# Performance work log

Hardware: AMD Instinct MI355X
Metric: run time of the kernel (lower is better)

## Reference

```python
import jax, jax.numpy as jnp
import numpy as np

N_NODES = 100000
N_EDGES = 3200000
DIMS = [32, 256, 1024, 1024, 256, 6]


def setup_inputs() -> dict:
    key = jax.random.key(0)
    ks = jax.random.split(key, 2 + 2 * 5)
    inp = {
        "x": jax.random.normal(ks[0], (N_NODES, DIMS[0]), dtype=jnp.float32),
        "edge_index": jax.random.randint(ks[1], (2, N_EDGES), 0, N_NODES, dtype=jnp.int64),
    }
    for i in range(5):
        fan_in, fan_out = DIMS[i], DIMS[i + 1]
        scale = (2.0 / (fan_in + fan_out)) ** 0.5  # glorot-ish
        inp[f"W{i+1}"] = jax.random.normal(ks[2 + 2 * i], (fan_in, fan_out), dtype=jnp.float32) * scale
        inp[f"b{i+1}"] = jnp.zeros((fan_out,), dtype=jnp.float32)
    return inp


def _gcn_forward(x, edge_index, Ws, bs):
    N = x.shape[0]
    # add self loops (PyG GCNConv default)
    loop = jnp.arange(N, dtype=edge_index.dtype)
    src = jnp.concatenate([edge_index[0], loop])
    dst = jnp.concatenate([edge_index[1], loop])
    # symmetric normalization: deg computed on target index (gcn_norm)
    deg = jax.ops.segment_sum(jnp.ones_like(dst, dtype=x.dtype), dst, num_segments=N)
    dinv = jnp.where(deg > 0, jax.lax.rsqrt(deg), 0.0)
    norm = (dinv[src] * dinv[dst])[:, None]  # [E+N, 1]

    def conv(h, W, b):
        h = h @ W                                    # dense linear
        msg = h[src] * norm                          # gather + scale
        agg = jax.ops.segment_sum(msg, dst, num_segments=N)  # scatter-add
        return agg + b

    h = x
    for i in range(4):
        h = jax.nn.relu(conv(h, Ws[i], bs[i]))
    return conv(h, Ws[4], bs[4])


def reference(x, edge_index, W1, b1, W2, b2, W3, b3, W4, b4, W5, b5):
    return _gcn_forward(x, edge_index, (W1, W2, W3, W4, W5), (b1, b2, b3, b4, b5))
```

## Files before the change

### kernel.cpp

```cpp
#include <hip/hip_runtime.h>

typedef unsigned char u8;
typedef unsigned short u16;
typedef unsigned int u32;
typedef __bf16 bf16_t;
typedef bf16_t bf16x8 __attribute__((ext_vector_type(8)));
typedef float f32x4 __attribute__((ext_vector_type(4)));
typedef float f32x2 __attribute__((ext_vector_type(2)));

#define LDS_PTR(p) ((__attribute__((address_space(3))) unsigned int*)(p))
#define GLB_PTR(p) ((const __attribute__((address_space(1))) unsigned int*)(p))

#define BSH 9
#define BCAP 32768

static __device__ __forceinline__ float bf2f(u16 h) {
  u32 u = ((u32)h) << 16;
  return __builtin_bit_cast(float, u);
}
static __device__ __forceinline__ u16 f2bf(float f) {
  u32 u = __builtin_bit_cast(u32, f);
  u += 0x7fffu + ((u >> 16) & 1u);
  return (u16)(u >> 16);
}

static __device__ __forceinline__ int xcd_swizzle(int wg, int nwg) {
  const int q = nwg >> 3, r = nwg & 7;
  const int xcd = wg & 7, pos = wg >> 3;
  return (xcd < r ? xcd * (q + 1) : r * (q + 1) + (xcd - r) * q) + pos;
}

__global__ void detect_kernel(const int* __restrict__ ei, const u16* __restrict__ x,
                              int* __restrict__ flags, int* __restrict__ zp, int zn) {
  __shared__ int cnt;
  if (threadIdx.x == 0) cnt = 0;
  __syncthreads();
  if (blockIdx.x == 0) {
    if (ei[1 + 2 * threadIdx.x] != 0) atomicAdd(&cnt, 1);
    __syncthreads();
    if (threadIdx.x == 0) flags[0] = (cnt == 0) ? 1 : 0;
  } else if (blockIdx.x == 1) {
    u32 u = x[threadIdx.x];
    u32 e = (u >> 7) & 0xFF;
    if (e >= 0x60 && e <= 0x83) atomicAdd(&cnt, 1);
    __syncthreads();
    if (threadIdx.x == 0) flags[1] = (cnt >= 240) ? 0 : 1;
  } else {
    for (int i = threadIdx.x; i < zn; i += 256) zp[i] = 0;
  }
}

static __device__ __forceinline__ int eidx(const void* ei, size_t i, int m) {
  return m ? (int)((const long long*)ei)[i] : ((const int*)ei)[i];
}

__global__ void zero_out_kernel(void* __restrict__ out, int n, const int* __restrict__ flags) {
  int i = blockIdx.x * 256 + threadIdx.x;
  if (i < n) {
    if (flags[1]) ((float*)out)[i] = 0.0f;
    else ((u16*)out)[i] = 0;
  }
}

struct CvtArgs {
  const void* src[10];
  u16* dst[10];
  int K[10];
  int N[10];
  int start[11];
};
__global__ void convert_all_kernel(CvtArgs a, const int* __restrict__ flags) {
  int idx = blockIdx.x * 256 + threadIdx.x;
  int f32 = flags[1];
#pragma unroll
  for (int t = 0; t < 10; ++t) {
    if (idx >= a.start[t] && idx < a.start[t + 1]) {
      int local = idx - a.start[t];
      int K = a.K[t], N = a.N[t];
      int k = local / N, n = local - k * N;
      float v = f32 ? ((const float*)a.src[t])[local] : bf2f(((const u16*)a.src[t])[local]);
      a.dst[t][(size_t)n * K + k] = f2bf(v);
    }
  }
}

__global__ __launch_bounds__(256) void bin_kernel(const void* __restrict__ ei,
                                                  int* __restrict__ gcur,
                                                  int2* __restrict__ pairs, int E, int Nn,
                                                  const int* __restrict__ flags, int nblk) {
  __shared__ int h[256];
  __shared__ int base[256];
  const int m = flags[0];
  const int nb = (Nn + (1 << BSH) - 1) >> BSH;
  const int per = (E + nblk - 1) / nblk;
  const int e0 = blockIdx.x * per;
  const int e1 = (e0 + per < E) ? e0 + per : E;
  for (int i = threadIdx.x; i < nb; i += 256) h[i] = 0;
  __syncthreads();
  for (int e = e0 + threadIdx.x; e < e1; e += 256) {
    int d = eidx(ei, (size_t)E + e, m);
    if ((u32)d < (u32)Nn) atomicAdd(&h[d >> BSH], 1);
  }
  __syncthreads();
  for (int i = threadIdx.x; i < nb; i += 256) {
    base[i] = atomicAdd(&gcur[i], h[i]);
    h[i] = 0;
  }
  __syncthreads();
  for (int e = e0 + threadIdx.x; e < e1; e += 256) {
    int d = eidx(ei, (size_t)E + e, m);
    if ((u32)d >= (u32)Nn) continue;
    int s = eidx(ei, (size_t)e, m);
    if ((u32)s >= (u32)Nn) s = 0;
    int b = d >> BSH;
    int p = base[b] + atomicAdd(&h[b], 1);
    if (p < BCAP) pairs[(size_t)b * BCAP + p] = make_int2(s, d);
  }
}

__global__ __launch_bounds__(256) void bucket_scan_kernel(const int* __restrict__ gcur,
                                                          int* __restrict__ gbase, int NB) {
  __shared__ int sd[256];
  int tid = threadIdx.x;
  int v = (tid < NB) ? gcur[tid] : 0;
  if (v > BCAP) v = BCAP;
  sd[tid] = v;
  __syncthreads();
  for (int s = 1; s < 256; s <<= 1) {
    int t = (tid >= s) ? sd[tid - s] : 0;
    __syncthreads();
    sd[tid] += t;
    __syncthreads();
  }
  if (tid < NB) gbase[tid] = sd[tid] - v;
}

__global__ __launch_bounds__(512) void bucket_finalize_kernel(
    const int2* __restrict__ pairs, const int* __restrict__ gcur,
    const int* __restrict__ gbase, int* __restrict__ rowp, float* __restrict__ dinv,
    int* __restrict__ csr, int Nn) {
  __shared__ int cnt[512];
  __shared__ int scn[512];
  const int b = blockIdx.x;
  const int n0 = b << BSH;
  const int tid = threadIdx.x;
  cnt[tid] = 0;
  __syncthreads();
  int tot = gcur[b];
  if (tot > BCAP) tot = BCAP;
  for (int i = tid; i < tot; i += 512) {
    int2 pr = pairs[(size_t)b * BCAP + i];
    atomicAdd(&cnt[pr.y - n0], 1);
  }
  __syncthreads();
  int myc = cnt[tid];
  scn[tid] = myc;
  __syncthreads();
  for (int s = 1; s < 512; s <<= 1) {
    int t = (tid >= s) ? scn[tid - s] : 0;
    __syncthreads();
    scn[tid] += t;
    __syncthreads();
  }
  const int node = n0 + tid;
  const int start = gbase[b] + scn[tid] - myc;
  if (node < Nn) {
    rowp[node] = start;
    dinv[node] = rsqrtf((float)(myc + 1));
    if (node == Nn - 1) rowp[Nn] = gbase[b] + scn[tid];
  }
  cnt[tid] = start;
  __syncthreads();
  for (int i = tid; i < tot; i += 512) {
    int2 pr = pairs[(size_t)b * BCAP + i];
    int p = atomicAdd(&cnt[pr.y - n0], 1);
    csr[p] = pr.x;
  }
}

template <int NPW, int ACT, bool SRCF, bool DSTF, bool EDGEW>
__global__ __launch_bounds__(256) void spmm_narrow_kernel(
    const void* __restrict__ Hb, void* __restrict__ Gb,
    const int* __restrict__ rowp, const int* __restrict__ csr,
    const float* __restrict__ dinv, const u16* __restrict__ bias,
    int relu, int Nn, int src_stride, int dst_stride, const int* __restrict__ flags) {
  constexpr int G = 64 / NPW;
  constexpr int B = 16;
  const int lane = threadIdx.x & 63;
  const int col = lane & (G - 1);
  const int node = blockIdx.x * 4 * NPW + (threadIdx.x >> 6) * NPW + (lane / G);
  const bool anode = node < Nn;
  const bool act = anode && (col < ACT);
  int sf32 = 0, of32 = 0;
  if (SRCF) sf32 = flags[1];
  if (DSTF) of32 = flags[1];
  const u16* Hs = (const u16*)Hb;
  const float* Hf = (const float*)Hb;

  int e0 = 0, cnt = 0;
  if (anode) {
    e0 = rowp[node];
    cnt = rowp[node + 1] - e0;
  }
  float acc = 0.0f;
  for (int jb = 0; jb < cnt; jb += B) {
    int s[B];
#pragma unroll
    for (int j = 0; j < B; ++j) {
      bool val = (jb + j) < cnt;
      s[j] = val ? csr[e0 + jb + j] : node;
    }
    float wv[B];
    if constexpr (EDGEW) {
#pragma unroll
      for (int j = 0; j < B; ++j) wv[j] = ((jb + j) < cnt) ? dinv[s[j]] : 0.0f;
    }
    float v[B];
#pragma unroll
    for (int j = 0; j < B; ++j) {
      bool val = act && ((jb + j) < cnt);
      size_t idx = (size_t)s[j] * src_stride + col;
      v[j] = val ? ((SRCF && sf32) ? Hf[idx] : bf2f(Hs[idx])) : 0.0f;
    }
#pragma unroll
    for (int j = 0; j < B; ++j) {
      if constexpr (EDGEW) acc += wv[j] * v[j];
      else acc += v[j];
    }
  }
  if (!act) return;
  const float wi = dinv[node];
  {
    size_t idx = (size_t)node * src_stride + col;
    float sv = (SRCF && sf32) ? Hf[idx] : bf2f(Hs[idx]);
    if constexpr (EDGEW) acc += wi * sv;
    else acc += sv;
  }
  float v = acc * wi;
  if (bias) v += bf2f(bias[col]);
  if (relu) v = fmaxf(v, 0.0f);
  size_t didx = (size_t)node * dst_stride + col;
  if (DSTF && of32) ((float*)Gb)[didx] = v;
  else ((u16*)Gb)[didx] = f2bf(v);
}

template <int W>
__global__ __launch_bounds__(256) void spmm_fp8_kernel(
    const u8* __restrict__ Hq, u16* __restrict__ Gout,
    const int* __restrict__ rowp, const int* __restrict__ csr,
    const float* __restrict__ dinv, int n0, int n1, int dst_stride) {
  constexpr int BPL = W / 64;
  constexpr int ND = BPL / 4;
  constexpr int B = (W == 1024) ? 8 : 16;
  const int lane = threadIdx.x & 63;
  const int node = __builtin_amdgcn_readfirstlane(n0 + blockIdx.x * 4 + (threadIdx.x >> 6));
  if (node >= n1) return;
  const int off = lane * BPL;
  f32x2 acc[2 * ND] = {};

  auto dec1 = [&](const u32* d) {
#pragma unroll
    for (int q = 0; q < ND; ++q) {
      f32x2 a = __builtin_amdgcn_cvt_pk_f32_fp8((int)d[q], false);
      f32x2 b = __builtin_amdgcn_cvt_pk_f32_fp8((int)d[q], true);
      acc[2 * q] += a;
      acc[2 * q + 1] += b;
    }
  };
  auto ldrow = [&](u32* v, int s) {
    const u8* p = Hq + (size_t)s * W + off;
    if constexpr (ND == 4) *(int4*)v = *(const int4*)p;
    else v[0] = *(const u32*)p;
  };

  const int e0 = rowp[node];
  const int cnt = rowp[node + 1] - e0;
  const int tot = cnt + 1;
  const int NB2 = (tot + B - 1) / B;
  const int NBF = NB2 - 1;

  u32 vA[B][ND], vB[B][ND];

  auto ldb_full = [&](u32 (*v)[ND], int k) {
    const int base = k * B;
    int s[B];
#pragma unroll
    for (int j = 0; j < B; ++j) s[j] = csr[e0 + base + j];
#pragma unroll
    for (int j = 0; j < B; ++j) ldrow(v[j], s[j]);
  };
  auto ldb_last = [&](u32 (*v)[ND]) {
    const int base = NBF * B;
#pragma unroll
    for (int j = 0; j < B; ++j) {
      const int i = base + j;
      if (i < tot) {
        int s = (i < cnt) ? csr[e0 + i] : node;
        ldrow(v[j], s);
      } else {
#pragma unroll
        for (int q = 0; q < ND; ++q) v[j][q] = 0u;
      }
    }
  };
  auto decfull = [&](u32 (*v)[ND]) {
#pragma unroll
    for (int j = 0; j < B; ++j) dec1(v[j]);
  };

  if (NB2 == 1) {
    ldb_last(vA);
    decfull(vA);
  } else {
    ldb_last(vA);
    ldb_full(vB, 0);
    int k = 1;
    while (k + 1 < NBF) {
      decfull(vA);
      ldb_full(vA, k);
      decfull(vB);
      ldb_full(vB, k + 1);
      k += 2;
    }
    if (k < NBF) {
      decfull(vA);
      ldb_full(vA, k);
      decfull(vB);
      decfull(vA);
    } else {
      decfull(vA);
      decfull(vB);
    }
  }

  const float wi = dinv[node];
  u32 d[2 * ND];
#pragma unroll
  for (int kk = 0; kk < 2 * ND; ++kk) {
    float v0 = acc[kk].x * wi, v1 = acc[kk].y * wi;
    d[kk] = (u32)f2bf(v0) | ((u32)f2bf(v1) << 16);
  }
  u16* gp = Gout + (size_t)(node - n0) * dst_stride + off;
  if constexpr (ND == 4) {
    ((int4*)gp)[0] = make_int4((int)d[0], (int)d[1], (int)d[2], (int)d[3]);
    ((int4*)gp)[1] = make_int4((int)d[4], (int)d[5], (int)d[6], (int)d[7]);
  } else {
    *(int2*)gp = make_int2((int)d[0], (int)d[1]);
  }
}

__global__ __launch_bounds__(256) void spmm_u8_kernel(
    const u8* __restrict__ Hq, u16* __restrict__ G,
    const int* __restrict__ rowp, const int* __restrict__ csr,
    const float* __restrict__ dinv, const u32* __restrict__ maxbits,
    const u16* __restrict__ bias, int relu, int Nn, int dst_stride) {
  constexpr int B = 16;
  const int lane = threadIdx.x & 63;
  const int node = __builtin_amdgcn_readfirstlane(blockIdx.x * 4 + (threadIdx.x >> 6));
  if (node >= Nn) return;
  const int off = lane * 4;
  float mx = __builtin_bit_cast(float, *maxbits);
  float sq = mx > 0.0f ? mx * (1.0f / 127.0f) : 0.0f;
  float a0 = 0.0f, a1 = 0.0f, a2 = 0.0f, a3 = 0.0f, wsum = 0.0f;

  auto dec1 = [&](u32 d, float w) {
    a0 += w * (float)(d & 0xffu);
    a1 += w * (float)((d >> 8) & 0xffu);
    a2 += w * (float)((d >> 16) & 0xffu);
    a3 += w * (float)(d >> 24);
    wsum += w;
  };
  auto ldrow = [&](u32* v, int s) { *v = *(const u32*)(Hq + (size_t)s * 256 + off); };

  const int e0 = rowp[node];
  const int cnt = rowp[node + 1] - e0;
  const int tot = cnt + 1;
  const int NB2 = (tot + B - 1) / B;
  const int NBF = NB2 - 1;

  u32 vA[B], vB[B];
  float wA[B], wB[B];

  auto ldb_full = [&](u32* v, float* wv, int k) {
    const int base = k * B;
    int s[B];
#pragma unroll
    for (int j = 0; j < B; ++j) s[j] = csr[e0 + base + j];
#pragma unroll
    for (int j = 0; j < B; ++j) wv[j] = dinv[s[j]];
#pragma unroll
    for (int j = 0; j < B; ++j) ldrow(&v[j], s[j]);
  };
  auto ldb_last = [&](u32* v, float* wv) {
    const int base = NBF * B;
#pragma unroll
    for (int j = 0; j < B; ++j) {
      const int i = base + j;
      if (i < tot) {
        int s = (i < cnt) ? csr[e0 + i] : node;
        wv[j] = dinv[s];
        ldrow(&v[j], s);
      } else {
        v[j] = 0u;
        wv[j] = 0.0f;
      }
    }
  };
  auto decfull = [&](u32* v, float* wv) {
#pragma unroll
    for (int j = 0; j < B; ++j) dec1(v[j], wv[j]);
  };

  if (NB2 == 1) {
    ldb_last(vA, wA);
    decfull(vA, wA);
  } else {
    ldb_last(vA, wA);
    ldb_full(vB, wB, 0);
    int k = 1;
    while (k + 1 < NBF) {
      decfull(vA, wA);
      ldb_full(vA, wA, k);
      decfull(vB, wB);
      ldb_full(vB, wB, k + 1);
      k += 2;
    }
    if (k < NBF) {
      decfull(vA, wA);
      ldb_full(vA, wA, k);
      decfull(vB, wB);
      decfull(vA, wA);
    } else {
      decfull(vA, wA);
      decfull(vB, wB);
    }
  }

  const float wi = dinv[node];
  float su[4] = {a0, a1, a2, a3};
  float vals[4];
#pragma unroll
  for (int k2 = 0; k2 < 4; ++k2) {
    float v = (su[k2] - 128.0f * wsum) * wi * sq;
    if (bias) v += bf2f(bias[off + k2]);
    if (relu) v = fmaxf(v, 0.0f);
    vals[k2] = v;
  }
  u32 d0 = (u32)f2bf(vals[0]) | ((u32)f2bf(vals[1]) << 16);
  u32 d1 = (u32)f2bf(vals[2]) | ((u32)f2bf(vals[3]) << 16);
  *(int2*)(G + (size_t)node * dst_stride + off) = make_int2((int)d0, (int)d1);
}

__global__ void quant_kernel(const u16* __restrict__ t4, u8* __restrict__ t4q,
                             const u32* __restrict__ maxbits, int n4) {
  int i = blockIdx.x * 256 + threadIdx.x;
  if (i >= n4) return;
  float mx = __builtin_bit_cast(float, *maxbits);
  float inv = mx > 0.0f ? 127.0f / mx : 0.0f;
  int2 v = ((const int2*)t4)[i];
  float f0 = bf2f((u16)(v.x & 0xffff)), f1 = bf2f((u16)((u32)v.x >> 16));
  float f2 = bf2f((u16)(v.y & 0xffff)), f3 = bf2f((u16)((u32)v.y >> 16));
  int q0 = (int)rintf(f0 * inv), q1 = (int)rintf(f1 * inv);
  int q2 = (int)rintf(f2 * inv), q3 = (int)rintf(f3 * inv);
  q0 = min(127, max(-127, q0)) + 128; q1 = min(127, max(-127, q1)) + 128;
  q2 = min(127, max(-127, q2)) + 128; q3 = min(127, max(-127, q3)) + 128;
  ((u32*)t4q)[i] = (u32)q0 | ((u32)q1 << 8) | ((u32)q2 << 16) | ((u32)q3 << 24);
}

__global__ __launch_bounds__(512) void gemm256_kernel(
    const u16* __restrict__ A, int lda, const u16* __restrict__ Bt, int ldb,
    u16* __restrict__ C, int ldc, const u16* __restrict__ bias,
    int M, int K, int relu, int fp8out, const float* __restrict__ rowscale) {
  extern __shared__ u16 lds[];
  u16* ldsA = lds;
  u16* ldsB = lds + 32768;
  const int tid = threadIdx.x;
  const int lane = tid & 63;
  const int wid = __builtin_amdgcn_readfirstlane(tid >> 6);
  const int wr = wid >> 2, wc = wid & 3;
  const int lr = lane & 15, lq = lane >> 4;
  const int gx = gridDim.x;
  int wg = blockIdx.y * gx + blockIdx.x;
  wg = xcd_swizzle(wg, gx * gridDim.y);
  const int m0 = (wg / gx) * 256, n0 = (wg % gx) * 256;

  f32x4 acc[8][4] = {};

  auto STAGE = [&](int b, int kb) {
#pragma unroll
    for (int it = 0; it < 4; ++it) {
      int slot = it * 512 + tid;
      int row = slot >> 3, blk = slot & 7;
      int gm = m0 + row;
      if (gm >= M) gm = M - 1;
      int gcol = kb * 64 + ((blk ^ (row & 7)) << 3);
      __builtin_amdgcn_global_load_lds(GLB_PTR(A + (size_t)gm * lda + gcol),
                                       LDS_PTR(ldsA + (size_t)b * 16384 + slot * 8), 16, 0, 0);
    }
#pragma unroll
    for (int it = 0; it < 4; ++it) {
      int slot = it * 512 + tid;
      int row = slot >> 3, blk = slot & 7;
      int gn = n0 + row;
      int gcol = kb * 64 + ((blk ^ (row & 7)) << 3);
      __builtin_amdgcn_global_load_lds(GLB_PTR(Bt + (size_t)gn * ldb + gcol),
                                       LDS_PTR(ldsB + (size_t)b * 16384 + slot * 8), 16, 0, 0);
    }
  };

  auto COMPUTE = [&](int b) {
    const u16* Ab = ldsA + (size_t)b * 16384;
    const u16* Bb = ldsB + (size_t)b * 16384;
#pragma unroll
    for (int ks = 0; ks < 2; ++ks) {
      bf16x8 af[8], bfr[4];
#pragma unroll
      for (int i = 0; i < 8; ++i) {
        int R = wr * 128 + i * 16 + lr;
        af[i] = *(const bf16x8*)(Ab + R * 64 + ((ks * 32 + lq * 8) ^ ((R & 7) << 3)));
      }
#pragma unroll
      for (int j = 0; j < 4; ++j) {
        int S = wc * 64 + j * 16 + lr;
        bfr[j] = *(const bf16x8*)(Bb + S * 64 + ((ks * 32 + lq * 8) ^ ((S & 7) << 3)));
      }
#pragma unroll
      for (int i = 0; i < 8; ++i)
#pragma unroll
        for (int j = 0; j < 4; ++j)
          acc[i][j] = __builtin_amdgcn_mfma_f32_16x16x32_bf16(af[i], bfr[j], acc[i][j], 0, 0, 0);
    }
  };

  const int nk = K >> 6;
  STAGE(0, 0);
  STAGE(1, 1);
  asm volatile("s_waitcnt vmcnt(8)" ::: "memory");
  __builtin_amdgcn_sched_barrier(0);
  __builtin_amdgcn_s_barrier();
  __builtin_amdgcn_sched_barrier(0);

  for (int k = 0; k < nk; ++k) {
    const int cur = k & 1;
    COMPUTE(cur);
    if (k + 1 < nk) {
      __builtin_amdgcn_sched_barrier(0);
      __builtin_amdgcn_s_barrier();
      __builtin_amdgcn_sched_barrier(0);
      if (k + 2 < nk) {
        STAGE(cur, k + 2);
        asm volatile("s_waitcnt vmcnt(8)" ::: "memory");
      } else {
        asm volatile("s_waitcnt vmcnt(0)" ::: "memory");
      }
      __builtin_amdgcn_sched_barrier(0);
      __builtin_amdgcn_s_barrier();
      __builtin_amdgcn_sched_barrier(0);
    }
  }

#pragma unroll
  for (int i = 0; i < 8; ++i) {
    f32x4 rs4;
    if (rowscale) {
      rs4 = *(const f32x4*)(rowscale + (m0 + wr * 128 + i * 16 + lq * 4));
    }
#pragma unroll
    for (int j = 0; j < 4; ++j) {
      int col = n0 + wc * 64 + j * 16 + lr;
      float bv = bias ? bf2f(bias[col]) : 0.0f;
#pragma unroll
      for (int r = 0; r < 4; ++r) {
        int row = m0 + wr * 128 + i * 16 + lq * 4 + r;
        if (row < M) {
          float v = acc[i][j][r] + bv;
          if (relu) v = fmaxf(v, 0.0f);
          if (rowscale) v *= rs4[r];
          if (fp8out) {
            int pk = __builtin_amdgcn_cvt_pk_fp8_f32(v, v, 0, false);
            ((u8*)C)[(size_t)row * ldc + col] = (u8)(pk & 0xff);
          } else {
            C[(size_t)row * ldc + col] = f2bf(v);
          }
        }
      }
    }
  }
}

__global__ __launch_bounds__(256) void gemm_fast_kernel(
    const u16* __restrict__ A, int lda, const u16* __restrict__ Bt,
    u16* __restrict__ C, int ldc, const u16* __restrict__ bias,
    int M, int N, int K, int relu, int fp8out, u32* __restrict__ maxout,
    const float* __restrict__ rowscale) {
  __shared__ __align__(16) u16 sA[128 * 64];
  __shared__ __align__(16) u16 sB[128 * 64];
  const int tid = threadIdx.x;
  const int lane = tid & 63;
  const int wave = __builtin_amdgcn_readfirstlane(tid >> 6);
  const int gx = gridDim.x;
  int wg = blockIdx.y * gx + blockIdx.x;
  wg = xcd_swizzle(wg, gx * gridDim.y);
  const int m0 = (wg / gx) * 128, n0 = (wg % gx) * 128;
  const int wm = (wave & 1) * 64, wn = (wave >> 1) * 64;
  const int lr = lane & 15, lq = lane >> 4;
  const int lrow = lane >> 3;
  const int lcol = (lane & 7) * 8;
  f32x4 acc[4][4] = {};

  for (int kb = 0; kb < K; kb += 64) {
#pragma unroll
    for (int it = 0; it < 4; ++it) {
      const int rbase = (it * 4 + wave) * 8;
      int gm = m0 + rbase + lrow;
      if (gm >= M) gm = M - 1;
      __builtin_amdgcn_global_load_lds(GLB_PTR(A + (size_t)gm * lda + kb + lcol),
                                       LDS_PTR(sA + rbase * 64), 16, 0, 0);
      const int gn = n0 + rbase + lrow;
      __builtin_amdgcn_global_load_lds(GLB_PTR(Bt + (size_t)gn * K + kb + lcol),
                                       LDS_PTR(sB + rbase * 64), 16, 0, 0);
    }
    __syncthreads();
#pragma unroll
    for (int ks = 0; ks < 2; ++ks) {
      bf16x8 af[4], bfr[4];
#pragma unroll
      for (int i = 0; i < 4; ++i)
        af[i] = *(const bf16x8*)(sA + (wm + i * 16 + lr) * 64 + ks * 32 + lq * 8);
#pragma unroll
      for (int i = 0; i < 4; ++i)
        bfr[i] = *(const bf16x8*)(sB + (wn + i * 16 + lr) * 64 + ks * 32 + lq * 8);
#pragma unroll
      for (int im = 0; im < 4; ++im)
#pragma unroll
        for (int in = 0; in < 4; ++in)
          acc[im][in] = __builtin_amdgcn_mfma_f32_16x16x32_bf16(af[im], bfr[in], acc[im][in], 0, 0, 0);
    }
    __syncthreads();
  }
  u32 mymax = 0;
#pragma unroll
  for (int im = 0; im < 4; ++im) {
    f32x4 rs4;
    if (rowscale) {
      rs4 = *(const f32x4*)(rowscale + (m0 + wm + im * 16 + lq * 4));
    }
#pragma unroll
    for (int in = 0; in < 4; ++in) {
      int col = n0 + wn + in * 16 + lr;
      float bv = bias ? bf2f(bias[col]) : 0.0f;
#pragma unroll
      for (int r = 0; r < 4; ++r) {
        int row = m0 + wm + im * 16 + lq * 4 + r;
        if (row < M) {
          float v = acc[im][in][r] + bv;
          if (relu) v = fmaxf(v, 0.0f);
          if (rowscale) v *= rs4[r];
          if (maxout) {
            u32 ab = __builtin_bit_cast(u32, v) & 0x7fffffffu;
            mymax = mymax > ab ? mymax : ab;
          }
          if (fp8out) {
            int pk = __builtin_amdgcn_cvt_pk_fp8_f32(v, v, 0, false);
            ((u8*)C)[(size_t)row * ldc + col] = (u8)(pk & 0xff);
          } else {
            C[(size_t)row * ldc + col] = f2bf(v);
          }
        }
      }
    }
  }
  if (maxout) {
    u32* red = (u32*)sA;
    red[tid] = mymax;
    __syncthreads();
    for (int s = 128; s > 0; s >>= 1) {
      if (tid < s) red[tid] = red[tid] > red[tid + s] ? red[tid] : red[tid + s];
      __syncthreads();
    }
    if (tid == 0) atomicMax(maxout, red[0]);
  }
}

#define LP 72
__global__ __launch_bounds__(256) void gemm_small_kernel(
    const u16* __restrict__ A, int lda, const u16* __restrict__ Bt,
    u16* __restrict__ C, int ldc, const u16* __restrict__ bias,
    int M, int N, int K, int relu, int fp8out, const float* __restrict__ rowscale) {
  __shared__ __align__(16) u16 sA[128 * LP];
  __shared__ __align__(16) u16 sB[128 * LP];
  const int tid = threadIdx.x;
  const int lane = tid & 63, wave = tid >> 6;
  const int gx = gridDim.x;
  int wg = blockIdx.y * gx + blockIdx.x;
  wg = xcd_swizzle(wg, gx * gridDim.y);
  const int m0 = (wg / gx) * 128, n0 = (wg % gx) * 128;
  const int wm = (wave & 1) * 64, wn = (wave >> 1) * 64;
  const int lr = lane & 15;
  const int lq = lane >> 4;
  f32x4 acc[4][4] = {};

  for (int kb = 0; kb < K; kb += 64) {
#pragma unroll
    for (int it = 0; it < 4; ++it) {
      int linear = it * 2048 + tid * 8;
      int row = linear >> 6, kc = linear & 63;
      int gm = m0 + row, gk = kb + kc;
      int4 v = make_int4(0, 0, 0, 0);
      if (gm < M && gk < K) v = *(const int4*)(A + (size_t)gm * lda + gk);
      *(int4*)(sA + row * LP + kc) = v;
    }
#pragma unroll
    for (int it = 0; it < 4; ++it) {
      int linear = it * 2048 + tid * 8;
      int row = linear >> 6, kc = linear & 63;
      int gn = n0 + row, gk = kb + kc;
      int4 v = make_int4(0, 0, 0, 0);
      if (gn < N && gk < K) v = *(const int4*)(Bt + (size_t)gn * K + gk);
      *(int4*)(sB + row * LP + kc) = v;
    }
    __syncthreads();
#pragma unroll
    for (int ks = 0; ks < 2; ++ks) {
      bf16x8 af[4], bfr[4];
#pragma unroll
      for (int i = 0; i < 4; ++i)
        af[i] = *(const bf16x8*)(sA + (wm + i * 16 + lr) * LP + ks * 32 + lq * 8);
#pragma unroll
      for (int i = 0; i < 4; ++i)
        bfr[i] = *(const bf16x8*)(sB + (wn + i * 16 + lr) * LP + ks * 32 + lq * 8);
#pragma unroll
      for (int im = 0; im < 4; ++im)
#pragma unroll
        for (int in = 0; in < 4; ++in)
          acc[im][in] = __builtin_amdgcn_mfma_f32_16x16x32_bf16(af[im], bfr[in], acc[im][in], 0, 0, 0);
    }
    __syncthreads();
  }
#pragma unroll
  for (int im = 0; im < 4; ++im) {
    f32x4 rs4;
    if (rowscale) rs4 = *(const f32x4*)(rowscale + (m0 + wm + im * 16 + lq * 4));
#pragma unroll
    for (int in = 0; in < 4; ++in) {
      int col = n0 + wn + in * 16 + lr;
      if (col >= N) continue;
      float bv = bias ? bf2f(bias[col]) : 0.0f;
#pragma unroll
      for (int r = 0; r < 4; ++r) {
        int row = m0 + wm + im * 16 + lq * 4 + r;
        if (row < M) {
          float v = acc[im][in][r] + bv;
          if (relu) v = fmaxf(v, 0.0f);
          if (rowscale) v *= rs4[r];
          if (fp8out) {
            int pk = __builtin_amdgcn_cvt_pk_fp8_f32(v, v, 0, false);
            ((u8*)C)[(size_t)row * ldc + col] = (u8)(pk & 0xff);
          } else {
            C[(size_t)row * ldc + col] = f2bf(v);
          }
        }
      }
    }
  }
}

extern "C" void kernel_launch(void* const* d_in, const int* in_sizes, int n_in,
                              void* d_out, int out_size, void* d_ws, size_t ws_size,
                              hipStream_t stream) {
  const u16* x  = (const u16*)d_in[0];
  const int* ei = (const int*)d_in[1];

  const int Nn = in_sizes[0] / 32;
  const int E  = in_sizes[1] / 2;
  const int NB = (Nn + (1 << BSH) - 1) >> BSH;

  char* w = (char*)d_ws;
  size_t off = 0;
  auto alloc = [&](size_t bytes) -> void* {
    void* p = w + off;
    off = (off + bytes + 255) & ~(size_t)255;
    return p;
  };
  int*   flags  = (int*)alloc(256);
  int*   gcur   = (int*)alloc(1024);
  int*   gbase  = (int*)alloc(1024);
  u32*   tmax   = (u32*)alloc(256);
  int*   rowp   = (int*)alloc((size_t)(Nn + 1) * 4);
  float* dinv   = (float*)alloc((size_t)Nn * 4);
  int*   csr    = (int*)alloc((size_t)E * 4);
  u16*   Wt1    = (u16*)alloc((size_t)32 * 256 * 2);
  u16*   Wt2    = (u16*)alloc((size_t)256 * 1024 * 2);
  u16*   Wt3    = (u16*)alloc((size_t)1024 * 1024 * 2);
  u16*   Wt4    = (u16*)alloc((size_t)1024 * 256 * 2);
  u16*   Wt5    = (u16*)alloc((size_t)256 * 6 * 2);
  u16*   bc1    = (u16*)alloc(256 * 2);
  u16*   bc2    = (u16*)alloc(1024 * 2);
  u16*   bc3    = (u16*)alloc(1024 * 2);
  u16*   bc4    = (u16*)alloc(256 * 2);
  u16*   bc5    = (u16*)alloc(6 * 2);

  const size_t fixed_end = off;
  const size_t hbytes = (size_t)Nn * 1024 * 2;
  auto align256 = [](size_t b) { return (b + 255) & ~(size_t)255; };
  int CH = Nn / 4;
  if (CH < 1) CH = 1;
  {
    size_t need = fixed_end + align256((size_t)CH * 1024 * 2) + align256(hbytes);
    if (ws_size < need) CH = (Nn + 7) / 8;
  }
  while ((size_t)CH * 1024 < (size_t)Nn * 32) CH *= 2;
  const int NR = (Nn + CH - 1) / CH;

  u16*   S      = (u16*)alloc((size_t)CH * 1024 * 2);
  u16*   H      = (u16*)alloc(hbytes);
  const size_t required = off;
  (void)n_in;

  if (ws_size < required) {
    if (ws_size >= 4096) {
      detect_kernel<<<3, 256, 0, stream>>>(ei, x, flags, gcur, 576);
      zero_out_kernel<<<(out_size + 255) / 256, 256, 0, stream>>>(d_out, out_size, flags);
    }
    return;
  }

  u8*  h2q = (u8*)H;
  u8*  t4q = (u8*)H;
  u16* g2  = H + (size_t)Nn * 512;
  u16* t4  = H + (size_t)Nn * 512;
  u8*  h1q = (u8*)(H + (size_t)Nn * 768);
  u16* h3R = H + (size_t)Nn * 768;
  u16* h4  = H + (size_t)Nn * 768;

  int2* pairs = (int2*)H;

  detect_kernel<<<3, 256, 0, stream>>>(ei, x, flags, gcur, 576);
  bin_kernel<<<1024, 256, 0, stream>>>(ei, gcur, pairs, E, Nn, flags, 1024);
  bucket_scan_kernel<<<1, 256, 0, stream>>>(gcur, gbase, NB);
  bucket_finalize_kernel<<<NB, 512, 0, stream>>>(pairs, gcur, gbase, rowp, dinv, csr, Nn);

  {
    CvtArgs a;
    const int Ks[10] = {32, 1, 256, 1, 1024, 1, 1024, 1, 256, 1};
    const int Ns[10] = {256, 256, 1024, 1024, 1024, 1024, 256, 256, 6, 6};
    u16* ds[10] = {Wt1, bc1, Wt2, bc2, Wt3, bc3, Wt4, bc4, Wt5, bc5};
    int cum = 0;
    for (int t = 0; t < 10; ++t) {
      a.src[t] = d_in[2 + t];
      a.dst[t] = ds[t];
      a.K[t] = Ks[t];
      a.N[t] = Ns[t];
      a.start[t] = cum;
      cum += Ks[t] * Ns[t];
    }
    a.start[10] = cum;
    convert_all_kernel<<<(cum + 255) / 256, 256, 0, stream>>>(a, flags);
  }

  const int sg = (Nn + 3) / 4;
  const int mb = (Nn + 127) / 128;

  (void)hipGetLastError();
  bool use256 = true;

  spmm_narrow_kernel<2, 32, true, false, true><<<(Nn + 7) / 8, 256, 0, stream>>>(
      x, S, rowp, csr, dinv, nullptr, 0, Nn, 32, 32, flags);
  gemm_small_kernel<<<dim3(2, mb), 256, 0, stream>>>(S, 32, Wt1, (u16*)h1q, 256, bc1,
                                                     Nn, 256, 32, 1, 1, dinv);

  spmm_fp8_kernel<256><<<sg, 256, 0, stream>>>(h1q, g2, rowp, csr, dinv, 0, Nn, 256);
  gemm_fast_kernel<<<dim3(8, mb), 256, 0, stream>>>(g2, 256, Wt2, (u16*)h2q, 1024, bc2,
                                                    Nn, 1024, 256, 1, 1, nullptr, dinv);

  for (int R = 0; R < NR; ++R) {
    int n0 = R * CH;
    int n1 = n0 + CH < Nn ? n0 + CH : Nn;
    int MR = n1 - n0;
    int mbr = (MR + 127) / 128;
    spmm_fp8_kernel<1024><<<(MR + 3) / 4, 256, 0, stream>>>(h2q, S, rowp, csr, dinv, n0, n1, 1024);
    if (use256) {
      int mtr = (MR + 255) / 256;
      gemm256_kernel<<<dim3(4, mtr), 512, 131072, stream>>>(S, 1024, Wt3, 1024, h3R, 1024,
                                                            bc3, MR, 1024, 1, 0, nullptr);
      if (hipGetLastError() != hipSuccess) use256 = false;
    }
    if (!use256) {
      gemm_fast_kernel<<<dim3(8, mbr), 256, 0, stream>>>(S, 1024, Wt3, h3R, 1024, bc3,
                                                         MR, 1024, 1024, 1, 0, nullptr, nullptr);
    }
    gemm_fast_kernel<<<dim3(2, mbr), 256, 0, stream>>>(h3R, 1024, Wt4, t4 + (size_t)n0 * 256, 256,
                                                       nullptr, MR, 256, 1024, 0, 0, tmax, nullptr);
  }

  quant_kernel<<<(Nn * 64 + 255) / 256, 256, 0, stream>>>(t4, t4q, tmax, Nn * 64);

  spmm_u8_kernel<<<sg, 256, 0, stream>>>(t4q, h4, rowp, csr, dinv, tmax, bc4, 1, Nn, 256);

  gemm_small_kernel<<<dim3(1, mb), 256, 0, stream>>>(h4, 256, Wt5, S, 6, nullptr,
                                                     Nn, 6, 256, 0, 0, nullptr);
  spmm_narrow_kernel<8, 6, false, true, true><<<(Nn + 31) / 32, 256, 0, stream>>>(
      S, d_out, rowp, csr, dinv, bc5, 0, Nn, 6, 6, flags);
}
```

Measured before the change: 1.979 ms.

## Add double-buffered direct-to-LDS GEMM for layer-2 linear, trim K loop in small GEMM

Adds a new GEMM kernel that stages A and B tiles straight into LDS with global_load_lds and double-buffers them, so the next K-tile loads while the current one feeds MFMA. It replaces the layer-2 GEMM (K=256, N=1024) and falls back to the old kernel if the launch fails. The small GEMM also skips the second k-substep when K is 32, avoiding MFMAs on zero padding. Costs are 64KB of dynamic LDS per block, which may reduce occupancy, and an unpadded LDS layout that may cause bank conflicts.

```diff
diff --git a/kernel.cpp b/kernel.cpp
--- a/kernel.cpp
+++ b/kernel.cpp
@@ -574,6 +574,101 @@
         int row = m0 + wr * 128 + i * 16 + lq * 4 + r;
         if (row < M) {
           float v = acc[i][j][r] + bv;
+          if (relu) v = fmaxf(v, 0.0f);
+          if (rowscale) v *= rs4[r];
+          if (fp8out) {
+            int pk = __builtin_amdgcn_cvt_pk_fp8_f32(v, v, 0, false);
+            ((u8*)C)[(size_t)row * ldc + col] = (u8)(pk & 0xff);
+          } else {
+            C[(size_t)row * ldc + col] = f2bf(v);
+          }
+        }
+      }
+    }
+  }
+}
+
+__global__ __launch_bounds__(256) void gemm_dbuf_kernel(
+    const u16* __restrict__ A, int lda, const u16* __restrict__ Bt,
+    u16* __restrict__ C, int ldc, const u16* __restrict__ bias,
+    int M, int N, int K, int relu, int fp8out, const float* __restrict__ rowscale) {
+  extern __shared__ u16 lds2[];
+  const int tid = threadIdx.x;
+  const int lane = tid & 63;
+  const int wave = __builtin_amdgcn_readfirstlane(tid >> 6);
+  const int gx = gridDim.x;
+  int wg = blockIdx.y * gx + blockIdx.x;
+  wg = xcd_swizzle(wg, gx * gridDim.y);
+  const int m0 = (wg / gx) * 128, n0 = (wg % gx) * 128;
+  const int wm = (wave & 1) * 64, wn = (wave >> 1) * 64;
+  const int lr = lane & 15, lq = lane >> 4;
+  const int lrow = lane >> 3;
+  const int lcol = (lane & 7) * 8;
+  f32x4 acc[4][4] = {};
+
+  auto STAGE = [&](int b, int kb) {
+#pragma unroll
+    for (int it = 0; it < 4; ++it) {
+      const int rbase = (it * 4 + wave) * 8;
+      int gm = m0 + rbase + lrow;
+      if (gm >= M) gm = M - 1;
+      __builtin_amdgcn_global_load_lds(GLB_PTR(A + (size_t)gm * lda + kb + lcol),
+                                       LDS_PTR(lds2 + b * 8192 + rbase * 64), 16, 0, 0);
+      const int gn = n0 + rbase + lrow;
+      __builtin_amdgcn_global_load_lds(GLB_PTR(Bt + (size_t)gn * K + kb + lcol),
+                                       LDS_PTR(lds2 + 16384 + b * 8192 + rbase * 64), 16, 0, 0);
+    }
+  };
+
+  const int nk = K >> 6;
+  STAGE(0, 0);
+  asm volatile("s_waitcnt vmcnt(0)" ::: "memory");
+  __builtin_amdgcn_sched_barrier(0);
+  __builtin_amdgcn_s_barrier();
+  __builtin_amdgcn_sched_barrier(0);
+
+  for (int t = 0; t < nk; ++t) {
+    const int cur = t & 1;
+    if (t + 1 < nk) STAGE(cur ^ 1, (t + 1) << 6);
+    const u16* Ab = lds2 + cur * 8192;
+    const u16* Bb = lds2 + 16384 + cur * 8192;
+#pragma unroll
+    for (int ks = 0; ks < 2; ++ks) {
+      bf16x8 af[4], bfr[4];
+#pragma unroll
+      for (int i = 0; i < 4; ++i)
+        af[i] = *(const bf16x8*)(Ab + (wm + i * 16 + lr) * 64 + ks * 32 + lq * 8);
+#pragma unroll
+      for (int i = 0; i < 4; ++i)
+        bfr[i] = *(const bf16x8*)(Bb + (wn + i * 16 + lr) * 64 + ks * 32 + lq * 8);
+#pragma unroll
+      for (int im = 0; im < 4; ++im)
+#pragma unroll
+        for (int in = 0; in < 4; ++in)
+          acc[im][in] = __builtin_amdgcn_mfma_f32_16x16x32_bf16(af[im], bfr[in], acc[im][in], 0, 0, 0);
+    }
+    if (t + 1 < nk) {
+      __builtin_amdgcn_sched_barrier(0);
+      asm volatile("s_waitcnt vmcnt(0)" ::: "memory");
+      __builtin_amdgcn_sched_barrier(0);
+      __builtin_amdgcn_s_barrier();
+      __builtin_amdgcn_sched_barrier(0);
+    }
+  }
+
+#pragma unroll
+  for (int im = 0; im < 4; ++im) {
+    f32x4 rs4;
+    if (rowscale) rs4 = *(const f32x4*)(rowscale + (m0 + wm + im * 16 + lq * 4));
+#pragma unroll
+    for (int in = 0; in < 4; ++in) {
+      int col = n0 + wn + in * 16 + lr;
+      float bv = bias ? bf2f(bias[col]) : 0.0f;
+#pragma unroll
+      for (int r = 0; r < 4; ++r) {
+        int row = m0 + wm + im * 16 + lq * 4 + r;
+        if (row < M) {
+          float v = acc[im][in][r] + bv;
           if (relu) v = fmaxf(v, 0.0f);
           if (rowscale) v *= rs4[r];
           if (fp8out) {
@@ -698,6 +793,7 @@
   const int wm = (wave & 1) * 64, wn = (wave >> 1) * 64;
   const int lr = lane & 15;
   const int lq = lane >> 4;
+  const int nks = (K > 32) ? 2 : 1;
   f32x4 acc[4][4] = {};
 
   for (int kb = 0; kb < K; kb += 64) {
@@ -720,8 +816,7 @@
       *(int4*)(sB + row * LP + kc) = v;
     }
     __syncthreads();
-#pragma unroll
-    for (int ks = 0; ks < 2; ++ks) {
+    for (int ks = 0; ks < nks; ++ks) {
       bf16x8 af[4], bfr[4];
 #pragma unroll
       for (int i = 0; i < 4; ++i)
@@ -870,8 +965,14 @@
                                                      Nn, 256, 32, 1, 1, dinv);
 
   spmm_fp8_kernel<256><<<sg, 256, 0, stream>>>(h1q, g2, rowp, csr, dinv, 0, Nn, 256);
-  gemm_fast_kernel<<<dim3(8, mb), 256, 0, stream>>>(g2, 256, Wt2, (u16*)h2q, 1024, bc2,
-                                                    Nn, 1024, 256, 1, 1, nullptr, dinv);
+  {
+    gemm_dbuf_kernel<<<dim3(8, mb), 256, 65536, stream>>>(g2, 256, Wt2, (u16*)h2q, 1024, bc2,
+                                                          Nn, 1024, 256, 1, 1, dinv);
+    if (hipGetLastError() != hipSuccess) {
+      gemm_fast_kernel<<<dim3(8, mb), 256, 0, stream>>>(g2, 256, Wt2, (u16*)h2q, 1024, bc2,
+                                                        Nn, 1024, 256, 1, 1, nullptr, dinv);
+    }
+  }
 
   for (int R = 0; R < NR; ++R) {
     int n0 = R * CH;
```

After: 2.040 ms. 1.03x slower.
